# Optimization experiments

Measured on AMD Instinct MI355X. Metric: run time of the kernel, lower is better.

## Reference

```python
import jax, jax.numpy as jnp
import numpy as np

B, N, F_IN, F_OUT = 8, 4096, 256, 256


def setup_inputs() -> dict:
    key = jax.random.key(0)
    k1, k2, k3 = jax.random.split(key, 3)
    H = jax.random.normal(k1, (B, N, F_IN), dtype=jnp.float32)
    W = jax.random.normal(k2, (F_IN, F_OUT), dtype=jnp.float32) * (1.0 / np.sqrt(F_IN))
    A = jax.random.normal(k3, (N, N), dtype=jnp.float32) * (1.414 * np.sqrt(2.0 / (N + N)))
    return {"H": H, "W": W, "A": A}


def reference(H, W, A):
    # HW: [B, N, F_out]
    HW = jnp.einsum('bnf,fo->bno', H, W)
    # symmetrize + relu -> nonneg adjacency [N, N]
    A_norm = jax.nn.relu((A + A.T) * 0.5)
    # degree and inverse sqrt (inf -> 0 for isolated nodes)
    D = jnp.sum(A_norm, axis=1)
    D_safe = jnp.where(D > 0, D, 1.0)
    d_inv_sqrt = jnp.where(D > 0, D_safe ** -0.5, 0.0)
    # L_norm = I - D^{-1/2} A D^{-1/2}  (diagonal scaling, no dense diag matmul)
    DAD = d_inv_sqrt[:, None] * A_norm * d_inv_sqrt[None, :]
    L_norm = jnp.eye(N, dtype=H.dtype) - DAD
    # output = relu(L_norm @ HW): [B, N, F_out]
    out = jnp.einsum('nm,bmo->bno', L_norm, HW)
    return jax.nn.relu(out)
```

## Files before the change

### kernel.cpp

```cpp
#include <hip/hip_runtime.h>
#include <stdint.h>

#define N_NODES 4096
#define F_DIM   256
#define BATCH   8

typedef __attribute__((ext_vector_type(8))) __bf16 bf16x8;
typedef __attribute__((ext_vector_type(4))) float  f32x4;
typedef __attribute__((ext_vector_type(8))) unsigned short u16x8;

typedef const __attribute__((address_space(1))) void* gas1_t;
typedef __attribute__((address_space(3))) void*       las3_t;

__device__ __forceinline__ void stage16(const void* g, void* l) {
  __builtin_amdgcn_global_load_lds((gas1_t)g, (las3_t)l, 16, 0, 0);
}

__device__ __forceinline__ unsigned short f2bf(float f) {
  union { float f; uint32_t u; } v; v.f = f;
  uint32_t u = v.u;
  return (unsigned short)((u + 0x7FFFu + ((u >> 16) & 1u)) >> 16);
}
__device__ __forceinline__ float bf2f(unsigned short u) {
  union { uint32_t u; float f; } v; v.u = ((uint32_t)u) << 16;
  return v.f;
}

__global__ __launch_bounds__(256) void k_pre(const float* __restrict__ A,
                                             unsigned short* __restrict__ Sb,
                                             float* __restrict__ D,
                                             const float4* __restrict__ H4,
                                             ushort4* __restrict__ Hb4,
                                             const float* __restrict__ W,
                                             unsigned short* __restrict__ Wt) {
  int t = threadIdx.x;
  int bid = blockIdx.y * 64 + blockIdx.x;
  {
    int i = bid * 512 + t;
    float4 v = H4[i];
    ushort4 o; o.x = f2bf(v.x); o.y = f2bf(v.y); o.z = f2bf(v.z); o.w = f2bf(v.w);
    Hb4[i] = o;
    i += 256;
    v = H4[i];
    o.x = f2bf(v.x); o.y = f2bf(v.y); o.z = f2bf(v.z); o.w = f2bf(v.w);
    Hb4[i] = o;
  }
  if (bid < 256) Wt[t * 256 + bid] = f2bf(W[bid * 256 + t]);

  int bi = blockIdx.y, bj = blockIdx.x;
  if (bj < bi) return;
  __shared__ float L1[64][65];
  __shared__ float L2[64][65];
  __shared__ float Pr[4][64];
  __shared__ float Pc[4][64];
  int i0 = bi * 64, j0 = bj * 64;
  for (int it = 0; it < 16; ++it) {
    int idx = it * 256 + t;
    int r = idx >> 6, c = idx & 63;
    L1[r][c] = A[(size_t)(i0 + r) * N_NODES + (j0 + c)];
    L2[c][r] = A[(size_t)(j0 + r) * N_NODES + (i0 + c)];
  }
  __syncthreads();
  float colsum = 0.f;
  int cfix = t & 63, q = t >> 6;
  for (int it = 0; it < 16; ++it) {
    int r = it * 4 + q;
    float v = 0.5f * (L1[r][cfix] + L2[r][cfix]);
    v = v > 0.f ? v : 0.f;
    Sb[(size_t)(i0 + r) * N_NODES + (j0 + cfix)] = f2bf(v);
    colsum += v;
    L1[r][cfix] = v;
  }
  Pc[q][cfix] = colsum;
  __syncthreads();
  {
    int r = t & 63, seg = t >> 6;
    float s = 0.f;
    for (int c = seg * 16; c < seg * 16 + 16; ++c) s += L1[r][c];
    Pr[seg][r] = s;
  }
  __syncthreads();
  if (t < 64) {
    float d = Pr[0][t] + Pr[1][t] + Pr[2][t] + Pr[3][t];
    atomicAdd(&D[i0 + t], d);
  } else if (t < 128 && bi != bj) {
    int c = t - 64;
    float d = Pc[0][c] + Pc[1][c] + Pc[2][c] + Pc[3][c];
    atomicAdd(&D[j0 + c], d);
  }
  if (bi != bj) {
    for (int it = 0; it < 16; ++it) {
      int idx = it * 256 + t;
      int ro = idx >> 6, co = idx & 63;
      Sb[(size_t)(j0 + ro) * N_NODES + (i0 + co)] = f2bf(L1[co][ro]);
    }
  }
}

__global__ void k_dinv(const float* __restrict__ D, float* __restrict__ dinv) {
  int i = blockIdx.x * blockDim.x + threadIdx.x;
  if (i < N_NODES) {
    float d = D[i];
    dinv[i] = d > 0.f ? 1.0f / sqrtf(d) : 0.f;
  }
}

__global__ __launch_bounds__(256) void k_gemm1(const unsigned short* __restrict__ Hb,
                                               const unsigned short* __restrict__ Wt,
                                               const float* __restrict__ dinv,
                                               unsigned short* __restrict__ HWb,
                                               unsigned short* __restrict__ Gt) {
  __shared__ __align__(16) unsigned short As[128 * 32];
  __shared__ __align__(16) unsigned short Bs[128 * 32];
  __shared__ __align__(16) unsigned short T[128][136];
  int t = threadIdx.x;
  int lane = t & 63;
  int q = lane >> 4, r16 = lane & 15;
  int wave = t >> 6;
  int wm = wave >> 1, wn = wave & 1;
  int m0 = blockIdx.y * 128;
  int o0 = blockIdx.x * 128;
  const int K = 256;

  const unsigned short* Abase = Hb + (size_t)m0 * K;
  const unsigned short* Bbase = Wt + (size_t)o0 * K;

  f32x4 acc[4][4];
#pragma unroll
  for (int i = 0; i < 4; ++i)
#pragma unroll
    for (int j = 0; j < 4; ++j) acc[i][j] = f32x4{0.f, 0.f, 0.f, 0.f};

  int idx0 = t, idx1 = 256 + t;
  int wb0 = (t & ~63) * 8;
  int wb1 = (256 + (t & ~63)) * 8;

  for (int kt = 0; kt < K / 32; ++kt) {
    int kof = kt * 32;
    stage16(Abase + (size_t)(idx0 >> 2) * K + kof + ((idx0 & 3) << 3), &As[wb0]);
    stage16(Abase + (size_t)(idx1 >> 2) * K + kof + ((idx1 & 3) << 3), &As[wb1]);
    stage16(Bbase + (size_t)(idx0 >> 2) * K + kof + ((idx0 & 3) << 3), &Bs[wb0]);
    stage16(Bbase + (size_t)(idx1 >> 2) * K + kof + ((idx1 & 3) << 3), &Bs[wb1]);
    __syncthreads();
    bf16x8 a[4], b[4];
#pragma unroll
    for (int mi = 0; mi < 4; ++mi)
      a[mi] = *(const bf16x8*)&As[(wm * 64 + mi * 16 + r16) * 32 + q * 8];
#pragma unroll
    for (int ni = 0; ni < 4; ++ni)
      b[ni] = *(const bf16x8*)&Bs[(wn * 64 + ni * 16 + r16) * 32 + q * 8];
#pragma unroll
    for (int mi = 0; mi < 4; ++mi)
#pragma unroll
      for (int ni = 0; ni < 4; ++ni)
        acc[mi][ni] = __builtin_amdgcn_mfma_f32_16x16x32_bf16(a[mi], b[ni], acc[mi][ni], 0, 0, 0);
    __syncthreads();
  }

#pragma unroll
  for (int mi = 0; mi < 4; ++mi) {
    int row = wm * 64 + mi * 16 + q * 4;
#pragma unroll
    for (int ni = 0; ni < 4; ++ni) {
      int col = wn * 64 + ni * 16 + r16;
#pragma unroll
      for (int rr = 0; rr < 4; ++rr) {
        unsigned short h = f2bf(acc[mi][ni][rr]);
        HWb[(size_t)(m0 + row + rr) * F_DIM + (o0 + col)] = h;
        T[col][row + rr] = h;
      }
    }
  }
  __syncthreads();
  int b = m0 >> 12, n0 = m0 & 4095;
  for (int it = 0; it < 8; ++it) {
    int unit = it * 256 + t;
    int ro = unit >> 4;
    int cs = (unit & 15) * 8;
    u16x8 v = *(const u16x8*)&T[ro][cs];
    u16x8 w;
#pragma unroll
    for (int j = 0; j < 8; ++j)
      w[j] = f2bf(bf2f(v[j]) * dinv[n0 + cs + j]);
    *(u16x8*)&Gt[(size_t)(b * 256 + o0 + ro) * N_NODES + n0 + cs] = w;
  }
}

__global__ __launch_bounds__(256, 2) void k_gemm2(const unsigned short* __restrict__ Sb,
                                                  const unsigned short* __restrict__ Gt,
                                                  const unsigned short* __restrict__ HWb,
                                                  const float* __restrict__ dinv,
                                                  float* __restrict__ Out) {
  __shared__ __align__(16) unsigned short As[128 * 32];
  __shared__ __align__(16) unsigned short Bs[128 * 32];
  __shared__ float Red[64 * 130];
  const int K = N_NODES;
  int t = threadIdx.x;
  int lane = t & 63;
  int q = lane >> 4, r16 = lane & 15;
  int wave = t >> 6;
  int wm = wave >> 1;
  int kz = wave & 1;

  int bid = blockIdx.y * 16 + blockIdx.x;
  int patch = bid & 7;
  int local = bid >> 3;
  int mt = (patch >> 1) * 8 + (local & 7);
  int nt = (patch & 1) * 8 + (local >> 3);
  int m0 = mt * 128;
  int n0 = nt * 128;

  const unsigned short* Abase = Sb + (size_t)m0 * K;
  const unsigned short* Bbase = Gt + (size_t)n0 * K;

  f32x4 acc[4][8];
#pragma unroll
  for (int i = 0; i < 4; ++i)
#pragma unroll
    for (int j = 0; j < 8; ++j) acc[i][j] = f32x4{0.f, 0.f, 0.f, 0.f};

  int u0 = t, u1 = 256 + t;
  int r0 = u0 >> 2, q0 = ((u0 & 3) - (r0 >> 1)) & 3;
  int r1 = u1 >> 2, q1 = ((u1 & 3) - (r1 >> 1)) & 3;
  const unsigned short* pa0 = Abase + (size_t)r0 * K + q0 * 8;
  const unsigned short* pa1 = Abase + (size_t)r1 * K + q1 * 8;
  const unsigned short* pb0 = Bbase + (size_t)r0 * K + q0 * 8;
  const unsigned short* pb1 = Bbase + (size_t)r1 * K + q1 * 8;
  int wb0 = (t & ~63) * 8;
  int wb1 = (256 + (t & ~63)) * 8;

  int aoff[4], boff[8];
#pragma unroll
  for (int mi = 0; mi < 4; ++mi) {
    int row = wm * 64 + mi * 16 + r16;
    aoff[mi] = row * 32 + (((q + (row >> 1)) & 3) << 3);
  }
#pragma unroll
  for (int ni = 0; ni < 8; ++ni) {
    int row = ni * 16 + r16;
    boff[ni] = row * 32 + (((q + (row >> 1)) & 3) << 3);
  }

  for (int kt = 0; kt < K / 32; ++kt) {
    int kof = kt * 32;
    stage16(pa0 + kof, &As[wb0]);
    stage16(pa1 + kof, &As[wb1]);
    stage16(pb0 + kof, &Bs[wb0]);
    stage16(pb1 + kof, &Bs[wb1]);
    __syncthreads();
    if ((kt & 1) == kz) {
      bf16x8 a[4], b[8];
#pragma unroll
      for (int mi = 0; mi < 4; ++mi) a[mi] = *(const bf16x8*)&As[aoff[mi]];
#pragma unroll
      for (int ni = 0; ni < 8; ++ni) b[ni] = *(const bf16x8*)&Bs[boff[ni]];
#pragma unroll
      for (int mi = 0; mi < 4; ++mi)
#pragma unroll
        for (int ni = 0; ni < 8; ++ni)
          acc[mi][ni] = __builtin_amdgcn_mfma_f32_16x16x32_bf16(a[mi], b[ni], acc[mi][ni], 0, 0, 0);
    }
    __syncthreads();
  }

  for (int round = 0; round < 2; ++round) {
    if (wm == round && kz == 1) {
#pragma unroll
      for (int mi = 0; mi < 4; ++mi)
#pragma unroll
        for (int ni = 0; ni < 8; ++ni)
#pragma unroll
          for (int rr = 0; rr < 4; ++rr)
            Red[(mi * 16 + q * 4 + rr) * 130 + ni * 16 + r16] = acc[mi][ni][rr];
    }
    __syncthreads();
    if (wm == round && kz == 0) {
#pragma unroll
      for (int mi = 0; mi < 4; ++mi) {
        int row = m0 + wm * 64 + mi * 16 + q * 4;
        float di[4];
#pragma unroll
        for (int rr = 0; rr < 4; ++rr) di[rr] = dinv[row + rr];
#pragma unroll
        for (int ni = 0; ni < 8; ++ni) {
          int col = n0 + ni * 16 + r16;
          int b_ = col >> 8, o = col & 255;
#pragma unroll
          for (int rr = 0; rr < 4; ++rr) {
            float v = acc[mi][ni][rr] + Red[(mi * 16 + q * 4 + rr) * 130 + ni * 16 + r16];
            size_t oi = ((size_t)b_ * N_NODES + (row + rr)) * F_DIM + o;
            float u = bf2f(HWb[oi]) - di[rr] * v;
            Out[oi] = u > 0.f ? u : 0.f;
          }
        }
      }
    }
    __syncthreads();
  }
}

extern "C" void kernel_launch(void* const* d_in, const int* in_sizes, int n_in,
                              void* d_out, int out_size, void* d_ws, size_t ws_size,
                              hipStream_t stream) {
  (void)in_sizes; (void)n_in; (void)out_size; (void)ws_size;
  const float* H = (const float*)d_in[0];
  const float* W = (const float*)d_in[1];
  const float* A = (const float*)d_in[2];
  float* out = (float*)d_out;

  char* ws = (char*)d_ws;
  size_t off = 0;
  auto alloc = [&](size_t bytes) {
    char* p = ws + off;
    off += (bytes + 255) & ~(size_t)255;
    return p;
  };
  float*          Dd   = (float*)alloc((size_t)N_NODES * 4);
  float*          dinv = (float*)alloc((size_t)N_NODES * 4);
  unsigned short* Sb   = (unsigned short*)alloc((size_t)N_NODES * N_NODES * 2);
  unsigned short* HWb  = (unsigned short*)alloc((size_t)BATCH * N_NODES * F_DIM * 2);
  unsigned short* Gt   = (unsigned short*)alloc((size_t)BATCH * F_DIM * N_NODES * 2);
  unsigned short* Wt   = (unsigned short*)alloc((size_t)F_DIM * F_DIM * 2);
  unsigned short* Hb   = (unsigned short*)alloc((size_t)BATCH * N_NODES * F_DIM * 2);

  hipMemsetAsync(Dd, 0, N_NODES * 4, stream);
  k_pre<<<dim3(64, 64), 256, 0, stream>>>(A, Sb, Dd, (const float4*)H, (ushort4*)Hb, W, Wt);
  k_dinv<<<16, 256, 0, stream>>>(Dd, dinv);
  k_gemm1<<<dim3(2, 256), 256, 0, stream>>>(Hb, Wt, dinv, HWb, Gt);
  k_gemm2<<<dim3(16, 32), 256, 0, stream>>>(Sb, Gt, HWb, dinv, out);
}
```

Measured before the change: 256.7 us.

## Double-buffer LDS tiles with K=64 steps in GEMM2 and shrink reduction buffer

The main GEMM loop now stages 64-wide K tiles into two LDS buffers, issuing the prefetch of the next tile before computing the current one. This replaces the two barriers per 32-wide step with a single barrier per 64-wide step and lets global-to-LDS loads overlap the MFMA work. The swizzle moves to an 8-chunk XOR-style rotation for the wider rows. The split-K reduction buffer shrinks to one 16-row slice per round, which means 8 rounds of barriers in the epilogue instead of 2. LDS use changes from about 49KB to about 74KB, which may limit how many blocks fit per CU.

```diff
diff --git a/kernel.cpp b/kernel.cpp
--- a/kernel.cpp
+++ b/kernel.cpp
@@ -191,10 +191,11 @@
                                                   const unsigned short* __restrict__ HWb,
                                                   const float* __restrict__ dinv,
                                                   float* __restrict__ Out) {
-  __shared__ __align__(16) unsigned short As[128 * 32];
-  __shared__ __align__(16) unsigned short Bs[128 * 32];
-  __shared__ float Red[64 * 130];
+  __shared__ __align__(16) unsigned short As[2][128 * 64];
+  __shared__ __align__(16) unsigned short Bs[2][128 * 64];
+  __shared__ float Red[16 * 132];
   const int K = N_NODES;
+  const int KT = K / 64;
   int t = threadIdx.x;
   int lane = t & 63;
   int q = lane >> 4, r16 = lane & 15;
@@ -219,79 +220,90 @@
 #pragma unroll
     for (int j = 0; j < 8; ++j) acc[i][j] = f32x4{0.f, 0.f, 0.f, 0.f};
 
-  int u0 = t, u1 = 256 + t;
-  int r0 = u0 >> 2, q0 = ((u0 & 3) - (r0 >> 1)) & 3;
-  int r1 = u1 >> 2, q1 = ((u1 & 3) - (r1 >> 1)) & 3;
-  const unsigned short* pa0 = Abase + (size_t)r0 * K + q0 * 8;
-  const unsigned short* pa1 = Abase + (size_t)r1 * K + q1 * 8;
-  const unsigned short* pb0 = Bbase + (size_t)r0 * K + q0 * 8;
-  const unsigned short* pb1 = Bbase + (size_t)r1 * K + q1 * 8;
-  int wb0 = (t & ~63) * 8;
-  int wb1 = (256 + (t & ~63)) * 8;
-
-  int aoff[4], boff[8];
-#pragma unroll
-  for (int mi = 0; mi < 4; ++mi) {
-    int row = wm * 64 + mi * 16 + r16;
-    aoff[mi] = row * 32 + (((q + (row >> 1)) & 3) << 3);
-  }
-#pragma unroll
-  for (int ni = 0; ni < 8; ++ni) {
-    int row = ni * 16 + r16;
-    boff[ni] = row * 32 + (((q + (row >> 1)) & 3) << 3);
-  }
-
-  for (int kt = 0; kt < K / 32; ++kt) {
-    int kof = kt * 32;
-    stage16(pa0 + kof, &As[wb0]);
-    stage16(pa1 + kof, &As[wb1]);
-    stage16(pb0 + kof, &Bs[wb0]);
-    stage16(pb1 + kof, &Bs[wb1]);
-    __syncthreads();
+  size_t gsrc[4];
+  int ldsu[4];
+#pragma unroll
+  for (int j = 0; j < 4; ++j) {
+    int s = j * 256 + t;
+    int row = s >> 3, up = s & 7;
+    int u = (up - row) & 7;
+    gsrc[j] = (size_t)row * K + u * 8;
+    ldsu[j] = (j * 256 + (t & ~63)) * 8;
+  }
+
+  int aoff[2][4], boff[2][8];
+#pragma unroll
+  for (int c = 0; c < 2; ++c) {
+#pragma unroll
+    for (int mi = 0; mi < 4; ++mi) {
+      int row = wm * 64 + mi * 16 + r16;
+      aoff[c][mi] = row * 64 + (((c * 4 + q + row) & 7) << 3);
+    }
+#pragma unroll
+    for (int ni = 0; ni < 8; ++ni) {
+      int row = ni * 16 + r16;
+      boff[c][ni] = row * 64 + (((c * 4 + q + row) & 7) << 3);
+    }
+  }
+
+#define STG(kt, bb)                                              \
+  {                                                              \
+    size_t kof = (size_t)(kt) * 64;                              \
+    _Pragma("unroll")                                            \
+    for (int j = 0; j < 4; ++j) {                                \
+      stage16(Abase + gsrc[j] + kof, &As[bb][ldsu[j]]);          \
+      stage16(Bbase + gsrc[j] + kof, &Bs[bb][ldsu[j]]);          \
+    }                                                            \
+  }
+
+  STG(0, 0)
+  for (int kt = 0; kt < KT; ++kt) {
+    int cur = kt & 1;
+    __syncthreads();
+    if (kt + 1 < KT) STG(kt + 1, cur ^ 1)
     if ((kt & 1) == kz) {
-      bf16x8 a[4], b[8];
-#pragma unroll
-      for (int mi = 0; mi < 4; ++mi) a[mi] = *(const bf16x8*)&As[aoff[mi]];
-#pragma unroll
-      for (int ni = 0; ni < 8; ++ni) b[ni] = *(const bf16x8*)&Bs[boff[ni]];
-#pragma unroll
-      for (int mi = 0; mi < 4; ++mi)
-#pragma unroll
-        for (int ni = 0; ni < 8; ++ni)
-          acc[mi][ni] = __builtin_amdgcn_mfma_f32_16x16x32_bf16(a[mi], b[ni], acc[mi][ni], 0, 0, 0);
-    }
-    __syncthreads();
-  }
-
-  for (int round = 0; round < 2; ++round) {
-    if (wm == round && kz == 1) {
-#pragma unroll
-      for (int mi = 0; mi < 4; ++mi)
-#pragma unroll
-        for (int ni = 0; ni < 8; ++ni)
-#pragma unroll
-          for (int rr = 0; rr < 4; ++rr)
-            Red[(mi * 16 + q * 4 + rr) * 130 + ni * 16 + r16] = acc[mi][ni][rr];
-    }
-    __syncthreads();
-    if (wm == round && kz == 0) {
-#pragma unroll
-      for (int mi = 0; mi < 4; ++mi) {
-        int row = m0 + wm * 64 + mi * 16 + q * 4;
-        float di[4];
-#pragma unroll
-        for (int rr = 0; rr < 4; ++rr) di[rr] = dinv[row + rr];
-#pragma unroll
-        for (int ni = 0; ni < 8; ++ni) {
-          int col = n0 + ni * 16 + r16;
-          int b_ = col >> 8, o = col & 255;
-#pragma unroll
-          for (int rr = 0; rr < 4; ++rr) {
-            float v = acc[mi][ni][rr] + Red[(mi * 16 + q * 4 + rr) * 130 + ni * 16 + r16];
-            size_t oi = ((size_t)b_ * N_NODES + (row + rr)) * F_DIM + o;
-            float u = bf2f(HWb[oi]) - di[rr] * v;
-            Out[oi] = u > 0.f ? u : 0.f;
-          }
+#pragma unroll
+      for (int c = 0; c < 2; ++c) {
+        bf16x8 a[4], b[8];
+#pragma unroll
+        for (int mi = 0; mi < 4; ++mi) a[mi] = *(const bf16x8*)&As[cur][aoff[c][mi]];
+#pragma unroll
+        for (int ni = 0; ni < 8; ++ni) b[ni] = *(const bf16x8*)&Bs[cur][boff[c][ni]];
+#pragma unroll
+        for (int mi = 0; mi < 4; ++mi)
+#pragma unroll
+          for (int ni = 0; ni < 8; ++ni)
+            acc[mi][ni] = __builtin_amdgcn_mfma_f32_16x16x32_bf16(a[mi], b[ni], acc[mi][ni], 0, 0, 0);
+      }
+    }
+  }
+#undef STG
+
+  for (int round = 0; round < 8; ++round) {
+    int half = round >> 2, mi = round & 3;
+    if (wm == half && kz == 1) {
+#pragma unroll
+      for (int ni = 0; ni < 8; ++ni)
+#pragma unroll
+        for (int rr = 0; rr < 4; ++rr)
+          Red[(q * 4 + rr) * 132 + ni * 16 + r16] = acc[mi][ni][rr];
+    }
+    __syncthreads();
+    if (wm == half && kz == 0) {
+      int row = m0 + wm * 64 + mi * 16 + q * 4;
+      float di[4];
+#pragma unroll
+      for (int rr = 0; rr < 4; ++rr) di[rr] = dinv[row + rr];
+#pragma unroll
+      for (int ni = 0; ni < 8; ++ni) {
+        int col = n0 + ni * 16 + r16;
+        int b_ = col >> 8, o = col & 255;
+#pragma unroll
+        for (int rr = 0; rr < 4; ++rr) {
+          float v = acc[mi][ni][rr] + Red[(q * 4 + rr) * 132 + ni * 16 + r16];
+          size_t oi = ((size_t)b_ * N_NODES + (row + rr)) * F_DIM + o;
+          float u = bf2f(HWb[oi]) - di[rr] * v;
+          Out[oi] = u > 0.f ? u : 0.f;
         }
       }
     }
```

Measured after the change: 557.3 us. 117% more time.
